# Optimization experiments

Hardware: AMD Instinct MI355X
Metric: run time of the kernel (lower is better)

The kernel has to match this reference:

```python
import jax, jax.numpy as jnp
import numpy as np

N = 4096          # N_TARGET_NODES (node count == feature dim)
E = 262144        # number of directed edges (avg degree 64)


def setup_inputs() -> dict:
    key = jax.random.key(0)
    k1, k2, k3, k4 = jax.random.split(key, 4)
    x = jax.random.normal(k1, (N, N), dtype=jnp.float32)
    edge_index = jax.random.randint(k2, (2, E), 0, N, dtype=jnp.int32)
    # scale weights so sigmoid inputs are O(1)
    W1 = jax.random.normal(k3, (N, N), dtype=jnp.float32) * (1.0 / np.sqrt(N))
    b1 = jnp.zeros((N,), dtype=jnp.float32)
    W2 = jax.random.normal(k4, (N, 1), dtype=jnp.float32) * (1.0 / np.sqrt(N))
    b2 = jnp.zeros((1,), dtype=jnp.float32)
    return {"x": x, "edge_index": edge_index, "W1": W1, "b1": b1, "W2": W2, "b2": b2}


def _gcn_conv(x, edge_index, W, b):
    """PyG GCNConv: h = D^{-1/2}(A+I)D^{-1/2} (x W) + b, edge weights = 1."""
    n = x.shape[0]
    h = x @ W                                   # [n, out]
    loop = jnp.arange(n, dtype=edge_index.dtype)
    src = jnp.concatenate([edge_index[0], loop])  # add self loops
    dst = jnp.concatenate([edge_index[1], loop])
    deg = jax.ops.segment_sum(jnp.ones_like(src, dtype=h.dtype), dst, num_segments=n)
    dinv = jnp.where(deg > 0, jax.lax.rsqrt(deg), 0.0)
    norm = dinv[src] * dinv[dst]                # [E+n]
    msg = h[src] * norm[:, None]                # gather + scale
    out = jax.ops.segment_sum(msg, dst, num_segments=n)  # scatter-add at targets
    return out + b


def reference(x, edge_index, W1, b1, W2, b2):
    # torch.squeeze(x) is a no-op for 2-D x
    x1 = jax.nn.sigmoid(_gcn_conv(x, edge_index, W1, b1))
    # F.dropout in eval mode is identity (deterministic reference)
    x2 = jax.nn.sigmoid(_gcn_conv(x1, edge_index, W2, b2))
    return x2  # [N, 1]
```

## Files before the change

### kernel.cpp

```cpp
#include <hip/hip_runtime.h>


typedef __attribute__((ext_vector_type(8))) short bf16x8;
typedef __attribute__((ext_vector_type(4))) float f32x4;

#define NN 4096
#define NT 64

__device__ __forceinline__ unsigned f2bf(float f) {
  unsigned u = __float_as_uint(f);
  return (u + 0x7FFFu + ((u >> 16) & 1u)) >> 16;
}

#define GLDS(g, l) __builtin_amdgcn_global_load_lds(                      \
    (const __attribute__((address_space(1))) void*)(g),                   \
    (__attribute__((address_space(3))) void*)(l), 16, 0, 0)


__global__ void init_deg_kernel(float* deg) {
  int v = blockIdx.x * 256 + threadIdx.x;
  if (v < NN) deg[v] = 1.0f;
}

__global__ void count_deg_kernel(const int* __restrict__ dst, int E, float* deg) {
  int e = blockIdx.x * 256 + threadIdx.x;
  if (e < E) atomicAdd(&deg[dst[e]], 1.0f);
}

__global__ void dinv_kernel(const float* __restrict__ deg, float* __restrict__ dinv) {
  int v = blockIdx.x * 256 + threadIdx.x;
  if (v < NN) dinv[v] = rsqrtf(deg[v]);
}

__global__ void diag_kernel(const float* __restrict__ dinv, float* __restrict__ S) {
  int v = blockIdx.x * 256 + threadIdx.x;
  if (v < NN) { float d = dinv[v]; S[(size_t)v * NN + v] = d * d; }
}

__global__ void scatter_S_kernel(const int* __restrict__ src, const int* __restrict__ dst,
                                 int E, const float* __restrict__ dinv, float* __restrict__ S) {
  int e = blockIdx.x * 256 + threadIdx.x;
  if (e < E) {
    int s = src[e], d = dst[e];
    atomicAdd(&S[(size_t)d * NN + s], dinv[s] * dinv[d]);
  }
}


__global__ void cast_kernel(const float* __restrict__ in, unsigned short* __restrict__ out, int n) {
  int i = (blockIdx.x * 256 + threadIdx.x) * 8;
  if (i >= n) return;
  const float4* p = (const float4*)(in + i);
  float4 a = p[0], b = p[1];
  uint4 o;
  o.x = f2bf(a.x) | (f2bf(a.y) << 16);
  o.y = f2bf(a.z) | (f2bf(a.w) << 16);
  o.z = f2bf(b.x) | (f2bf(b.y) << 16);
  o.w = f2bf(b.z) | (f2bf(b.w) << 16);
  *(uint4*)(out + i) = o;
}

__global__ void transpose_cast_kernel(const float* __restrict__ W, unsigned short* __restrict__ WT) {
  __shared__ float tile[32][33];
  int bx = blockIdx.x * 32, by = blockIdx.y * 32;
  int tx = threadIdx.x, ty = threadIdx.y;
#pragma unroll
  for (int i = 0; i < 32; i += 8)
    tile[ty + i][tx] = W[(size_t)(by + ty + i) * NN + bx + tx];
  __syncthreads();
#pragma unroll
  for (int i = 0; i < 32; i += 8)
    WT[(size_t)(bx + ty + i) * NN + by + tx] = (unsigned short)f2bf(tile[tx][ty + i]);
}


template <int EPI>
__global__ __launch_bounds__(512, 2) void gemm256_kernel(
    const unsigned short* __restrict__ A, const unsigned short* __restrict__ BT,
    unsigned short* __restrict__ C, const float* __restrict__ bias) {
  __shared__ __align__(16) char smem[131072];
  const int tid = threadIdx.x;
  const int lane = tid & 63, wid = tid >> 6;
  const int wr = wid >> 2, wc = wid & 3;

  const int bid = blockIdx.x;
  const int swz = (bid & 7) * 32 + (bid >> 3);
  const int rowBase = (swz >> 4) * 256;
  const int colBase = (swz & 15) * 256;

  const int srow = tid >> 3;
  const int scolb = ((tid & 7) << 4) ^ ((srow & 7) << 4);
  const unsigned short* pA = A + (size_t)(rowBase + srow) * NN + (scolb >> 1);
  const unsigned short* pB = BT + (size_t)(colBase + srow) * NN + (scolb >> 1);
  char* ldsw = smem + (wid << 10);

  const int rl = lane & 15;
  const int c0 = ((lane >> 4) << 4) ^ ((lane & 7) << 4);
  const int c1 = c0 ^ 64;
  const int aoff = (wr * 128 + rl) * 128;
  const int boff = 32768 + (wc * 64 + rl) * 128;

  f32x4 acc[8][4] = {};

  GLDS(pB + (size_t)0 * 64 * NN, ldsw + 32768 + 0 * 8192);
  GLDS(pB + (size_t)1 * 64 * NN, ldsw + 32768 + 1 * 8192);
  GLDS(pB + (size_t)2 * 64 * NN, ldsw + 32768 + 2 * 8192);
  GLDS(pB + (size_t)3 * 64 * NN, ldsw + 32768 + 3 * 8192);
  GLDS(pA + (size_t)0 * 64 * NN, ldsw + 0 * 8192);
  GLDS(pA + (size_t)2 * 64 * NN, ldsw + 2 * 8192);
  GLDS(pA + (size_t)1 * 64 * NN, ldsw + 1 * 8192);
  GLDS(pA + (size_t)3 * 64 * NN, ldsw + 3 * 8192);
  asm volatile("s_waitcnt vmcnt(2)" ::: "memory");
  __builtin_amdgcn_s_barrier();

  for (int t = 0; t < NT; ++t) {
    const int cur = (t & 1) << 16;
    const char* lb = smem + cur;
    char* stw = ldsw + (cur ^ 65536);
    const unsigned short* sA = pA + (t + 1) * 64;
    const unsigned short* sB = pB + (t + 1) * 64;

    bf16x8 af[4], bk0[4], bk1[4];

#pragma unroll
    for (int m = 0; m < 4; ++m) af[m] = *(const bf16x8*)(lb + aoff + m * 2048 + c0);
#pragma unroll
    for (int n = 0; n < 4; ++n) bk0[n] = *(const bf16x8*)(lb + boff + n * 2048 + c0);
    GLDS(sB + (size_t)0 * 64 * NN, stw + 32768 + 0 * 8192);
    GLDS(sB + (size_t)1 * 64 * NN, stw + 32768 + 1 * 8192);
    __builtin_amdgcn_s_barrier();
    asm volatile("s_waitcnt lgkmcnt(0)" ::: "memory");
    __builtin_amdgcn_sched_barrier(0);
    __builtin_amdgcn_s_setprio(1);
#pragma unroll
    for (int m = 0; m < 4; ++m)
#pragma unroll
      for (int n = 0; n < 4; ++n)
        acc[m][n] = __builtin_amdgcn_mfma_f32_16x16x32_bf16(af[m], bk0[n], acc[m][n], 0, 0, 0);
    __builtin_amdgcn_s_setprio(0);
    __builtin_amdgcn_s_barrier();

#pragma unroll
    for (int m = 0; m < 4; ++m) af[m] = *(const bf16x8*)(lb + aoff + m * 2048 + c1);
#pragma unroll
    for (int n = 0; n < 4; ++n) bk1[n] = *(const bf16x8*)(lb + boff + n * 2048 + c1);
    GLDS(sB + (size_t)2 * 64 * NN, stw + 32768 + 2 * 8192);
    GLDS(sB + (size_t)3 * 64 * NN, stw + 32768 + 3 * 8192);
    asm volatile("s_waitcnt vmcnt(4)" ::: "memory");
    __builtin_amdgcn_s_barrier();
    asm volatile("s_waitcnt lgkmcnt(0)" ::: "memory");
    __builtin_amdgcn_sched_barrier(0);
    __builtin_amdgcn_s_setprio(1);
#pragma unroll
    for (int m = 0; m < 4; ++m)
#pragma unroll
      for (int n = 0; n < 4; ++n)
        acc[m][n] = __builtin_amdgcn_mfma_f32_16x16x32_bf16(af[m], bk1[n], acc[m][n], 0, 0, 0);
    __builtin_amdgcn_s_setprio(0);
    __builtin_amdgcn_s_barrier();

#pragma unroll
    for (int m = 0; m < 4; ++m) af[m] = *(const bf16x8*)(lb + aoff + (4 + m) * 2048 + c0);
    GLDS(sA + (size_t)0 * 64 * NN, stw + 0 * 8192);
    GLDS(sA + (size_t)2 * 64 * NN, stw + 2 * 8192);
    __builtin_amdgcn_s_barrier();
    asm volatile("s_waitcnt lgkmcnt(0)" ::: "memory");
    __builtin_amdgcn_sched_barrier(0);
    __builtin_amdgcn_s_setprio(1);
#pragma unroll
    for (int m = 0; m < 4; ++m)
#pragma unroll
      for (int n = 0; n < 4; ++n)
        acc[4 + m][n] = __builtin_amdgcn_mfma_f32_16x16x32_bf16(af[m], bk0[n], acc[4 + m][n], 0, 0, 0);
    __builtin_amdgcn_s_setprio(0);
    __builtin_amdgcn_s_barrier();

#pragma unroll
    for (int m = 0; m < 4; ++m) af[m] = *(const bf16x8*)(lb + aoff + (4 + m) * 2048 + c1);
    GLDS(sA + (size_t)1 * 64 * NN, stw + 1 * 8192);
    GLDS(sA + (size_t)3 * 64 * NN, stw + 3 * 8192);
    asm volatile("s_waitcnt vmcnt(2)" ::: "memory");
    __builtin_amdgcn_s_barrier();
    asm volatile("s_waitcnt lgkmcnt(0)" ::: "memory");
    __builtin_amdgcn_sched_barrier(0);
    __builtin_amdgcn_s_setprio(1);
#pragma unroll
    for (int m = 0; m < 4; ++m)
#pragma unroll
      for (int n = 0; n < 4; ++n)
        acc[4 + m][n] = __builtin_amdgcn_mfma_f32_16x16x32_bf16(af[m], bk1[n], acc[4 + m][n], 0, 0, 0);
    __builtin_amdgcn_s_setprio(0);
    __builtin_amdgcn_s_barrier();
  }

  const int orow = rowBase + wr * 128 + (lane >> 4) * 4;
  const int ocol = colBase + wc * 64 + (lane & 15);
#pragma unroll
  for (int n = 0; n < 4; ++n) {
    int ccol = ocol + n * 16;
    float bv = (EPI == 1) ? bias[ccol] : 0.0f;
#pragma unroll
    for (int m = 0; m < 8; ++m) {
#pragma unroll
      for (int i = 0; i < 4; ++i) {
        float x = acc[m][n][i] + bv;
        if (EPI == 1) x = 1.0f / (1.0f + __expf(-x));
        C[(size_t)(orow + m * 16 + i) * NN + ccol] = (unsigned short)f2bf(x);
      }
    }
  }
}


__global__ void matvec_kernel(const unsigned short* __restrict__ X1,
                              const float* __restrict__ W2, float* __restrict__ h2) {
  int row = blockIdx.x, t = threadIdx.x;
  const unsigned short* xr = X1 + (size_t)row * NN;
  float s = 0.0f;
  for (int j = t * 8; j < NN; j += 2048) {
    uint4 u = *(const uint4*)(xr + j);
    unsigned v[4] = {u.x, u.y, u.z, u.w};
#pragma unroll
    for (int q = 0; q < 4; ++q) {
      float lo = __uint_as_float(v[q] << 16);
      float hi = __uint_as_float(v[q] & 0xFFFF0000u);
      s += lo * W2[j + q * 2] + hi * W2[j + q * 2 + 1];
    }
  }
#pragma unroll
  for (int off = 32; off > 0; off >>= 1) s += __shfl_down(s, off);
  __shared__ float wsum[4];
  if ((t & 63) == 0) wsum[t >> 6] = s;
  __syncthreads();
  if (t == 0) h2[row] = wsum[0] + wsum[1] + wsum[2] + wsum[3];
}

__global__ void init_t_kernel(const float* __restrict__ dinv, const float* __restrict__ h2,
                              const float* __restrict__ b2, float* __restrict__ tacc) {
  int v = blockIdx.x * 256 + threadIdx.x;
  if (v < NN) tacc[v] = dinv[v] * dinv[v] * h2[v] + b2[0];
}

__global__ void scatter_t_kernel(const int* __restrict__ src, const int* __restrict__ dst,
                                 int E, const float* __restrict__ dinv,
                                 const float* __restrict__ h2, float* __restrict__ tacc) {
  int e = blockIdx.x * 256 + threadIdx.x;
  if (e < E) {
    int s = src[e], d = dst[e];
    atomicAdd(&tacc[d], dinv[s] * dinv[d] * h2[s]);
  }
}

__global__ void final_kernel(const float* __restrict__ tacc, float* __restrict__ out) {
  int v = blockIdx.x * 256 + threadIdx.x;
  if (v < NN) out[v] = 1.0f / (1.0f + __expf(-tacc[v]));
}


extern "C" void kernel_launch(void* const* d_in, const int* in_sizes, int n_in,
                              void* d_out, int out_size, void* d_ws, size_t ws_size,
                              hipStream_t stream) {
  const float* x  = (const float*)d_in[0];
  const int*   ei = (const int*)d_in[1];
  const float* W1 = (const float*)d_in[2];
  const float* b1 = (const float*)d_in[3];
  const float* W2 = (const float*)d_in[4];
  const float* b2 = (const float*)d_in[5];
  float* out = (float*)d_out;
  const int E = in_sizes[1] / 2;
  const int* esrc = ei;
  const int* edst = ei + E;

  char* w = (char*)d_ws;
  float*          Sf  = (float*)w;
  unsigned short* H1T = (unsigned short*)w;
  unsigned short* W1T = (unsigned short*)(w + (size_t)(32u << 20));
  unsigned short* Sbf = (unsigned short*)(w + (size_t)(64u << 20));
  unsigned short* Xbf = (unsigned short*)(w + (size_t)(96u << 20));
  float* deg  = (float*)(w + (size_t)(128u << 20));
  float* dinv = deg + 4096;
  float* h2   = deg + 8192;
  float* tacc = deg + 12288;

  init_deg_kernel<<<16, 256, 0, stream>>>(deg);
  count_deg_kernel<<<(E + 255) / 256, 256, 0, stream>>>(edst, E, deg);
  dinv_kernel<<<16, 256, 0, stream>>>(deg, dinv);

  hipMemsetAsync(Sf, 0, (size_t)64 << 20, stream);
  diag_kernel<<<16, 256, 0, stream>>>(dinv, Sf);
  scatter_S_kernel<<<(E + 255) / 256, 256, 0, stream>>>(esrc, edst, E, dinv, Sf);
  cast_kernel<<<8192, 256, 0, stream>>>(Sf, Sbf, NN * NN);

  cast_kernel<<<8192, 256, 0, stream>>>(x, Xbf, NN * NN);
  transpose_cast_kernel<<<dim3(128, 128), dim3(32, 8), 0, stream>>>(W1, W1T);

  gemm256_kernel<0><<<256, 512, 0, stream>>>(W1T, Xbf, H1T, nullptr);
  gemm256_kernel<1><<<256, 512, 0, stream>>>(Sbf, H1T, Xbf, b1);

  matvec_kernel<<<4096, 256, 0, stream>>>(Xbf, W2, h2);
  init_t_kernel<<<16, 256, 0, stream>>>(dinv, h2, b2, tacc);
  scatter_t_kernel<<<(E + 255) / 256, 256, 0, stream>>>(esrc, edst, E, dinv, h2, tacc);
  final_kernel<<<16, 256, 0, stream>>>(tacc, out);
}
```

Baseline: 381.4 us.

## Deepen GEMM global-to-LDS prefetch by staging A tiles two iterations ahead

```diff
diff --git a/kernel.cpp b/kernel.cpp
--- a/kernel.cpp
+++ b/kernel.cpp
@@ -92,7 +92,6 @@
   const int scolb = ((tid & 7) << 4) ^ ((srow & 7) << 4);
   const unsigned short* pA = A + (size_t)(rowBase + srow) * NN + (scolb >> 1);
   const unsigned short* pB = BT + (size_t)(colBase + srow) * NN + (scolb >> 1);
-  char* ldsw = smem + (wid << 10);
 
   const int rl = lane & 15;
   const int c0 = ((lane >> 4) << 4) ^ ((lane & 7) << 4);
@@ -102,23 +101,31 @@
 
   f32x4 acc[8][4] = {};
 
-  GLDS(pB + (size_t)0 * 64 * NN, ldsw + 32768 + 0 * 8192);
-  GLDS(pB + (size_t)1 * 64 * NN, ldsw + 32768 + 1 * 8192);
-  GLDS(pB + (size_t)2 * 64 * NN, ldsw + 32768 + 2 * 8192);
-  GLDS(pB + (size_t)3 * 64 * NN, ldsw + 32768 + 3 * 8192);
-  GLDS(pA + (size_t)0 * 64 * NN, ldsw + 0 * 8192);
-  GLDS(pA + (size_t)2 * 64 * NN, ldsw + 2 * 8192);
-  GLDS(pA + (size_t)1 * 64 * NN, ldsw + 1 * 8192);
-  GLDS(pA + (size_t)3 * 64 * NN, ldsw + 3 * 8192);
-  asm volatile("s_waitcnt vmcnt(2)" ::: "memory");
-  __builtin_amdgcn_s_barrier();
+  {
+    char* w0 = smem + (wid << 10);
+    char* w1 = smem + 65536 + (wid << 10);
+    GLDS(pB + (size_t)0 * 64 * NN, w0 + 32768 + 0 * 8192);
+    GLDS(pB + (size_t)1 * 64 * NN, w0 + 32768 + 1 * 8192);
+    GLDS(pB + (size_t)2 * 64 * NN, w0 + 32768 + 2 * 8192);
+    GLDS(pB + (size_t)3 * 64 * NN, w0 + 32768 + 3 * 8192);
+    GLDS(pA + (size_t)0 * 64 * NN, w0 + 0 * 8192);
+    GLDS(pA + (size_t)2 * 64 * NN, w0 + 2 * 8192);
+    GLDS(pA + (size_t)1 * 64 * NN, w0 + 1 * 8192);
+    GLDS(pA + (size_t)3 * 64 * NN, w0 + 3 * 8192);
+    GLDS(pA + 64 + (size_t)0 * 64 * NN, w1 + 0 * 8192);
+    GLDS(pA + 64 + (size_t)2 * 64 * NN, w1 + 2 * 8192);
+    asm volatile("s_waitcnt vmcnt(2)" ::: "memory");
+    __builtin_amdgcn_s_barrier();
+  }
 
   for (int t = 0; t < NT; ++t) {
     const int cur = (t & 1) << 16;
     const char* lb = smem + cur;
-    char* stw = ldsw + (cur ^ 65536);
-    const unsigned short* sA = pA + (t + 1) * 64;
-    const unsigned short* sB = pB + (t + 1) * 64;
+    char* stN = smem + (cur ^ 65536) + (wid << 10);
+    char* stC = smem + cur + (wid << 10);
+    const unsigned short* s1A = pA + ((t + 1) & 63) * 64;
+    const unsigned short* s1B = pB + ((t + 1) & 63) * 64;
+    const unsigned short* s2A = pA + ((t + 2) & 63) * 64;
 
     bf16x8 af[4], bk0[4], bk1[4];
 
@@ -126,8 +133,8 @@
     for (int m = 0; m < 4; ++m) af[m] = *(const bf16x8*)(lb + aoff + m * 2048 + c0);
 #pragma unroll
     for (int n = 0; n < 4; ++n) bk0[n] = *(const bf16x8*)(lb + boff + n * 2048 + c0);
-    GLDS(sB + (size_t)0 * 64 * NN, stw + 32768 + 0 * 8192);
-    GLDS(sB + (size_t)1 * 64 * NN, stw + 32768 + 1 * 8192);
+    GLDS(s1B + (size_t)0 * 64 * NN, stN + 32768 + 0 * 8192);
+    GLDS(s1B + (size_t)1 * 64 * NN, stN + 32768 + 1 * 8192);
     __builtin_amdgcn_s_barrier();
     asm volatile("s_waitcnt lgkmcnt(0)" ::: "memory");
     __builtin_amdgcn_sched_barrier(0);
@@ -144,9 +151,8 @@
     for (int m = 0; m < 4; ++m) af[m] = *(const bf16x8*)(lb + aoff + m * 2048 + c1);
 #pragma unroll
     for (int n = 0; n < 4; ++n) bk1[n] = *(const bf16x8*)(lb + boff + n * 2048 + c1);
-    GLDS(sB + (size_t)2 * 64 * NN, stw + 32768 + 2 * 8192);
-    GLDS(sB + (size_t)3 * 64 * NN, stw + 32768 + 3 * 8192);
-    asm volatile("s_waitcnt vmcnt(4)" ::: "memory");
+    GLDS(s1B + (size_t)2 * 64 * NN, stN + 32768 + 2 * 8192);
+    GLDS(s1B + (size_t)3 * 64 * NN, stN + 32768 + 3 * 8192);
     __builtin_amdgcn_s_barrier();
     asm volatile("s_waitcnt lgkmcnt(0)" ::: "memory");
     __builtin_amdgcn_sched_barrier(0);
@@ -157,12 +163,13 @@
       for (int n = 0; n < 4; ++n)
         acc[m][n] = __builtin_amdgcn_mfma_f32_16x16x32_bf16(af[m], bk1[n], acc[m][n], 0, 0, 0);
     __builtin_amdgcn_s_setprio(0);
+    asm volatile("s_waitcnt vmcnt(6)" ::: "memory");
     __builtin_amdgcn_s_barrier();
 
 #pragma unroll
     for (int m = 0; m < 4; ++m) af[m] = *(const bf16x8*)(lb + aoff + (4 + m) * 2048 + c0);
-    GLDS(sA + (size_t)0 * 64 * NN, stw + 0 * 8192);
-    GLDS(sA + (size_t)2 * 64 * NN, stw + 2 * 8192);
+    GLDS(s1A + (size_t)1 * 64 * NN, stN + 1 * 8192);
+    GLDS(s1A + (size_t)3 * 64 * NN, stN + 3 * 8192);
     __builtin_amdgcn_s_barrier();
     asm volatile("s_waitcnt lgkmcnt(0)" ::: "memory");
     __builtin_amdgcn_sched_barrier(0);
@@ -177,9 +184,8 @@
 
 #pragma unroll
     for (int m = 0; m < 4; ++m) af[m] = *(const bf16x8*)(lb + aoff + (4 + m) * 2048 + c1);
-    GLDS(sA + (size_t)1 * 64 * NN, stw + 1 * 8192);
-    GLDS(sA + (size_t)3 * 64 * NN, stw + 3 * 8192);
-    asm volatile("s_waitcnt vmcnt(2)" ::: "memory");
+    GLDS(s2A + (size_t)0 * 64 * NN, stC + 0 * 8192);
+    GLDS(s2A + (size_t)2 * 64 * NN, stC + 2 * 8192);
     __builtin_amdgcn_s_barrier();
     asm volatile("s_waitcnt lgkmcnt(0)" ::: "memory");
     __builtin_amdgcn_sched_barrier(0);
@@ -190,6 +196,7 @@
       for (int n = 0; n < 4; ++n)
         acc[4 + m][n] = __builtin_amdgcn_mfma_f32_16x16x32_bf16(af[m], bk1[n], acc[4 + m][n], 0, 0, 0);
     __builtin_amdgcn_s_setprio(0);
+    asm volatile("s_waitcnt vmcnt(4)" ::: "memory");
     __builtin_amdgcn_s_barrier();
   }
 
```

New measurement: 367.0 us. -3.8%, faster.
